# Optimization experiments

Hardware: AMD Instinct MI355X
Metric: run time of the kernel (lower is better)

## Reference

```python
import jax, jax.numpy as jnp
import numpy as np
from jax import lax

DIM = 64
HEADS = 8
B, H, W = 4, 256, 256


def layer_norm(x, w, b):
    # WithBias LayerNorm over channel dim (dim=1 of NCHW), per-pixel
    mu = jnp.mean(x, axis=1, keepdims=True)
    var = jnp.mean((x - mu) ** 2, axis=1, keepdims=True)
    xn = (x - mu) / jnp.sqrt(var + 1e-5)
    return xn * w[None, :, None, None] + b[None, :, None, None]


def conv1x1(x, w, b=None):
    out = jnp.einsum('oc,bchw->bohw', w, x)
    if b is not None:
        out = out + b[None, :, None, None]
    return out


def dwconv3x3(x, w):
    # w: [C,1,3,3], depthwise (groups=C), stride 1, pad 1
    return lax.conv_general_dilated(
        x, w, window_strides=(1, 1), padding=((1, 1), (1, 1)),
        feature_group_count=x.shape[1],
        dimension_numbers=('NCHW', 'OIHW', 'NCHW'))


def modulation(v, y, mw, mb):
    # mw: [4, C, C] = [scale0, scale1, shift0, shift1]; mb: [4, C]
    s = conv1x1(jax.nn.leaky_relu(conv1x1(y, mw[0], mb[0]), 0.1), mw[1], mb[1])
    t = conv1x1(jax.nn.leaky_relu(conv1x1(y, mw[2], mb[2]), 0.1), mw[3], mb[3])
    return v * (s + 1.0) + t


def _heads(t):
    b, c, h, w = t.shape
    return t.reshape(b, HEADS, c // HEADS, h * w)


def channel_attn(q, k, v, temp):
    b, c, h, w = v.shape
    q, k, v = _heads(q), _heads(k), _heads(v)  # b, head, ch, hw
    q = q / jnp.maximum(jnp.linalg.norm(q, axis=-1, keepdims=True), 1e-12)
    k = k / jnp.maximum(jnp.linalg.norm(k, axis=-1, keepdims=True), 1e-12)
    attn = jnp.einsum('bhcn,bhdn->bhcd', q, k) * temp[None]  # small CxC
    attn = jax.nn.softmax(attn, axis=-1)
    out = jnp.einsum('bhcd,bhdn->bhcn', attn, v)
    return out.reshape(b, c, h, w)


def setup_inputs() -> dict:
    key = jax.random.key(0)
    ks = jax.random.split(key, 24)
    sc = 0.05
    d = {
        'x': jax.random.normal(ks[0], (B, DIM, H, W), jnp.float32),
        'y': jax.random.normal(ks[1], (B, DIM, H, W), jnp.float32),
        'ln_w': jnp.ones((DIM,), jnp.float32),
        'ln_b': jnp.zeros((DIM,), jnp.float32),
        'temp': jnp.ones((HEADS, 1, 1), jnp.float32),
        'kv1_w': jax.random.normal(ks[2], (2 * DIM, DIM), jnp.float32) * sc,
        'kvdw1_w': jax.random.normal(ks[3], (2 * DIM, 1, 3, 3), jnp.float32) * sc,
        'q1_w': jax.random.normal(ks[4], (DIM, DIM), jnp.float32) * sc,
        'qdw1_w': jax.random.normal(ks[5], (DIM, 1, 3, 3), jnp.float32) * sc,
        'po1_w': jax.random.normal(ks[6], (DIM, DIM), jnp.float32) * sc,
        'kv2_w': jax.random.normal(ks[7], (2 * DIM, DIM), jnp.float32) * sc,
        'kvdw2_w': jax.random.normal(ks[8], (2 * DIM, 1, 3, 3), jnp.float32) * sc,
        'q2_w': jax.random.normal(ks[9], (DIM, DIM), jnp.float32) * sc,
        'qdw2_w': jax.random.normal(ks[10], (DIM, 1, 3, 3), jnp.float32) * sc,
        'po2_w': jax.random.normal(ks[11], (DIM, DIM), jnp.float32) * sc,
        'mm1_w': jax.random.normal(ks[12], (4, DIM, DIM), jnp.float32) * sc,
        'mm1_b': jnp.zeros((4, DIM), jnp.float32),
        'mm2_w': jax.random.normal(ks[13], (4, DIM, DIM), jnp.float32) * sc,
        'mm2_b': jnp.zeros((4, DIM), jnp.float32),
    }
    return d


def reference(x, y, ln_w, ln_b, temp,
              kv1_w, kvdw1_w, q1_w, qdw1_w, po1_w,
              kv2_w, kvdw2_w, q2_w, qdw2_w, po2_w,
              mm1_w, mm1_b, mm2_w, mm2_b):
    x1 = layer_norm(x, ln_w, ln_b)
    y1 = layer_norm(y, ln_w, ln_b)  # original reuses self.norm1 for both

    # branch 1: kv from x1, q from y1, v modulated by x, residual y
    kv1 = dwconv3x3(conv1x1(x1, kv1_w), kvdw1_w)
    k1, v1 = jnp.split(kv1, 2, axis=1)
    q1 = dwconv3x3(conv1x1(y1, q1_w), qdw1_w)
    v1 = modulation(v1, x, mm1_w, mm1_b)
    out1 = conv1x1(channel_attn(q1, k1, v1, temp), po1_w) + y

    # branch 2: kv from y1, q from x1, v modulated by y, residual x
    kv2 = dwconv3x3(conv1x1(y1, kv2_w), kvdw2_w)
    k2, v2 = jnp.split(kv2, 2, axis=1)
    q2 = dwconv3x3(conv1x1(x1, q2_w), qdw2_w)
    v2 = modulation(v2, y, mm2_w, mm2_b)
    out2 = conv1x1(channel_attn(q2, k2, v2, temp), po2_w) + x

    return (out1, out2)
```

## Files before the change

### kernel.cpp

```cpp
#include <hip/hip_runtime.h>
#include <hip/hip_bf16.h>

#define HW 65536
#define BATCH 4
#define NPIX (BATCH*HW)

typedef unsigned short u16;
typedef unsigned int   u32;
typedef __attribute__((ext_vector_type(8))) short bh8;
typedef __attribute__((ext_vector_type(4))) float f4;

__device__ __forceinline__ float b2f(u16 u){
    u32 i = ((u32)u) << 16; float f; __builtin_memcpy(&f, &i, 4); return f;
}
__device__ __forceinline__ u16 f2b(float f){
    __hip_bfloat16 h = __float2bfloat16(f); u16 u; __builtin_memcpy(&u, &h, 2); return u;
}

__device__ __forceinline__ f4 mfma16(bh8 a, bh8 b, f4 c){
    return __builtin_amdgcn_mfma_f32_16x16x32_bf16(a, b, c, 0, 0, 0);
}

struct CvtJob { const float* src; u16* dst; int n; const float* cs; };
struct CvtJobs { CvtJob j[12]; };
__global__ void cvt_kernel(CvtJobs jobs){
    const CvtJob J = jobs.j[blockIdx.x];
    if (J.cs){
        for (int i = threadIdx.x; i < J.n; i += 256) J.dst[i] = f2b(J.src[i] * J.cs[i & 63]);
    } else {
        for (int i = threadIdx.x; i < J.n; i += 256) J.dst[i] = f2b(J.src[i]);
    }
}

__global__ __launch_bounds__(256) void prep_kernel(const float* __restrict__ kv0w,
                                                   const float* __restrict__ kv1w,
                                                   const float* __restrict__ q0w,
                                                   const float* __restrict__ q1w,
                                                   const float* __restrict__ lnw,
                                                   const float* __restrict__ lnb,
                                                   float* __restrict__ sums,
                                                   float* __restrict__ lnc){
    int blk = blockIdx.x;
    if (blk == 0){
        for (int i = threadIdx.x; i < 5120; i += 256) sums[i] = 0.f;
    } else if (blk <= 2){
        const float* W = (blk == 1) ? kv0w : kv1w;
        float* rs = lnc + (blk-1)*256;
        int o = threadIdx.x;
        if (o < 128){
            float a = 0.f, bb = 0.f;
            for (int c = 0; c < 64; c++){
                float wv = W[o*64 + c];
                a = fmaf(wv, lnw[c], a); bb = fmaf(wv, lnb[c], bb);
            }
            rs[o] = a; rs[128 + o] = bb;
        }
    } else {
        const float* W = (blk == 3) ? q0w : q1w;
        float* rs = lnc + 512 + (blk-3)*128;
        int o = threadIdx.x;
        if (o < 64){
            float a = 0.f, bb = 0.f;
            for (int c = 0; c < 64; c++){
                float wv = W[o*64 + c];
                a = fmaf(wv, lnw[c], a); bb = fmaf(wv, lnb[c], bb);
            }
            rs[o] = a; rs[64 + o] = bb;
        }
    }
}

template<int MT, int KT, int EPI, typename TB, bool LNF>
__global__ __launch_bounds__(256) void gemm_kernel(
        const TB* __restrict__ inLo, const TB* __restrict__ inHi,
        const u16* __restrict__ WA,
        const float* __restrict__ rs, const float* __restrict__ rb,
        u16* __restrict__ outLo, u16* __restrict__ outHi,
        const float* __restrict__ resid, float* __restrict__ outF){
    constexpr int KD = KT*32;
    int tile = blockIdx.x;
    int w = threadIdx.x >> 6, lane = threadIdx.x & 63;
    int quad = lane >> 4, l16 = lane & 15;
    int b = tile >> 9;
    int pbase = ((tile & 511) << 7) + (w << 5) + (l16 << 1);

    bh8 a[MT][KT];
    const u16* wbase = (EPI == 3) ? (WA + b*4096) : WA;
    #pragma unroll
    for (int mi = 0; mi < MT; mi++){
        int row = mi*16 + l16;
        #pragma unroll
        for (int ks = 0; ks < KT; ks++)
            __builtin_memcpy(&a[mi][ks], wbase + row*KD + ks*32 + quad*8, 16);
    }
    f4 acc[MT][2];
    #pragma unroll
    for (int mi = 0; mi < MT; mi++){ acc[mi][0] = (f4){0.f,0.f,0.f,0.f}; acc[mi][1] = (f4){0.f,0.f,0.f,0.f}; }

    float s1a = 0.f, s2a = 0.f, s1b = 0.f, s2b = 0.f;
    #pragma unroll
    for (int ks = 0; ks < KT; ks++){
        int kblk = ks*32 + quad*8;
        const TB* base = (kblk < 64) ? inLo : inHi;
        const TB* pp = base + ((size_t)b*64 + (kblk & 63))*HW + pbase;
        bh8 b0, b1;
        #pragma unroll
        for (int j = 0; j < 8; j++){
            if constexpr (sizeof(TB) == 2){
                u32 m = *(const u32*)(pp + (size_t)j*HW);
                b0[j] = (short)(m & 0xffffu);
                b1[j] = (short)(m >> 16);
            } else {
                float2 f = *(const float2*)(pp + (size_t)j*HW);
                if constexpr (LNF){
                    s1a += f.x; s2a = fmaf(f.x, f.x, s2a);
                    s1b += f.y; s2b = fmaf(f.y, f.y, s2b);
                }
                b0[j] = (short)f2b(f.x);
                b1[j] = (short)f2b(f.y);
            }
        }
        #pragma unroll
        for (int mi = 0; mi < MT; mi++){
            acc[mi][0] = mfma16(a[mi][ks], b0, acc[mi][0]);
            acc[mi][1] = mfma16(a[mi][ks], b1, acc[mi][1]);
        }
    }

    float mu0 = 0.f, iv0 = 1.f, mu1 = 0.f, iv1 = 1.f;
    if constexpr (LNF){
        s1a += __shfl_xor(s1a, 16); s1a += __shfl_xor(s1a, 32);
        s2a += __shfl_xor(s2a, 16); s2a += __shfl_xor(s2a, 32);
        s1b += __shfl_xor(s1b, 16); s1b += __shfl_xor(s1b, 32);
        s2b += __shfl_xor(s2b, 16); s2b += __shfl_xor(s2b, 32);
        mu0 = s1a*(1.f/64.f); iv0 = rsqrtf(s2a*(1.f/64.f) - mu0*mu0 + 1e-5f);
        mu1 = s1b*(1.f/64.f); iv1 = rsqrtf(s2b*(1.f/64.f) - mu1*mu1 + 1e-5f);
    }

    #pragma unroll
    for (int mi = 0; mi < MT; mi++)
    #pragma unroll
    for (int r = 0; r < 4; r++){
        int o = mi*16 + quad*4 + r;
        size_t pidx = ((size_t)b*64 + (o & 63))*HW + pbase;
        float va0 = acc[mi][0][r];
        float va1 = acc[mi][1][r];
        if constexpr (EPI == 3){
            float2 rr = *(const float2*)(resid + pidx);
            float2 st; st.x = va0 + rr.x; st.y = va1 + rr.y;
            *(float2*)(outF + pidx) = st;
        } else {
            if constexpr (LNF){
                float rsv = rs[o], rbv = rb[o];
                va0 = iv0*(va0 - mu0*rsv) + rbv;
                va1 = iv1*(va1 - mu1*rsv) + rbv;
            }
            u16* dst = (o < 64) ? outLo : outHi;
            *(u32*)(dst + pidx) = (u32)f2b(va0) | ((u32)f2b(va1) << 16);
        }
    }
}

__global__ __launch_bounds__(256) void modfused_kernel(
        const float* __restrict__ in,
        const u16* __restrict__ WA, const u16* __restrict__ WB,
        const float* __restrict__ b0v, const float* __restrict__ b2v,
        const float* __restrict__ b1v, const float* __restrict__ b3v,
        u16* __restrict__ vP){
    __shared__ u32 lds[128*65];
    int tile = blockIdx.x;
    int w = threadIdx.x >> 6, lane = threadIdx.x & 63;
    int quad = lane >> 4, l16 = lane & 15;
    int b = tile >> 9;
    int pbase = ((tile & 511) << 7) + (w << 5) + (l16 << 1);
    int pxp = (w << 4) + l16;

    bh8 a1[8][2];
    #pragma unroll
    for (int mi = 0; mi < 8; mi++)
        #pragma unroll
        for (int ks = 0; ks < 2; ks++)
            __builtin_memcpy(&a1[mi][ks], WA + (mi*16+l16)*64 + ks*32 + quad*8, 16);
    f4 acc[8][2];
    #pragma unroll
    for (int mi = 0; mi < 8; mi++){ acc[mi][0] = (f4){0.f,0.f,0.f,0.f}; acc[mi][1] = (f4){0.f,0.f,0.f,0.f}; }
    #pragma unroll
    for (int ks = 0; ks < 2; ks++){
        const float* pp = in + ((size_t)b*64 + ks*32 + quad*8)*HW + pbase;
        bh8 f0, f1;
        #pragma unroll
        for (int j = 0; j < 8; j++){
            float2 f = *(const float2*)(pp + (size_t)j*HW);
            f0[j] = (short)f2b(f.x);
            f1[j] = (short)f2b(f.y);
        }
        #pragma unroll
        for (int mi = 0; mi < 8; mi++){
            acc[mi][0] = mfma16(a1[mi][ks], f0, acc[mi][0]);
            acc[mi][1] = mfma16(a1[mi][ks], f1, acc[mi][1]);
        }
    }
    #pragma unroll
    for (int mi = 0; mi < 8; mi++)
    #pragma unroll
    for (int r = 0; r < 4; r++){
        int o = mi*16 + quad*4 + r;
        float bi = (o < 64) ? b0v[o] : b2v[o-64];
        float v0 = acc[mi][0][r] + bi; v0 = v0 > 0.f ? v0 : 0.1f*v0;
        float v1 = acc[mi][1][r] + bi; v1 = v1 > 0.f ? v1 : 0.1f*v1;
        lds[o*65 + ((pxp + ((o>>2)&3)*4) & 63)] = (u32)f2b(v0) | ((u32)f2b(v1) << 16);
    }
    __syncthreads();

    bh8 a2[8][2];
    #pragma unroll
    for (int mi = 0; mi < 8; mi++)
        #pragma unroll
        for (int ks = 0; ks < 2; ks++)
            __builtin_memcpy(&a2[mi][ks], WB + (mi*16+l16)*64 + ks*32 + quad*8, 16);
    f4 acc2[8][2];
    #pragma unroll
    for (int mi = 0; mi < 8; mi++){ acc2[mi][0] = (f4){0.f,0.f,0.f,0.f}; acc2[mi][1] = (f4){0.f,0.f,0.f,0.f}; }
    #pragma unroll
    for (int ks = 0; ks < 4; ks++){
        int kb = ks*32 + quad*8;
        bh8 bb0, bb1;
        #pragma unroll
        for (int j = 0; j < 8; j++){
            int ch = kb + j;
            u32 m = lds[ch*65 + ((pxp + ((ch>>2)&3)*4) & 63)];
            bb0[j] = (short)(m & 0xffffu);
            bb1[j] = (short)(m >> 16);
        }
        #pragma unroll
        for (int mi = 0; mi < 8; mi++){
            if (mi < 4 ? (ks < 2) : (ks >= 2)){
                int ksl = (mi >= 4) ? ks - 2 : ks;
                acc2[mi][0] = mfma16(a2[mi][ksl], bb0, acc2[mi][0]);
                acc2[mi][1] = mfma16(a2[mi][ksl], bb1, acc2[mi][1]);
            }
        }
    }
    #pragma unroll
    for (int mi = 0; mi < 4; mi++)
    #pragma unroll
    for (int r = 0; r < 4; r++){
        int o = mi*16 + quad*4 + r;
        size_t pidx = ((size_t)b*64 + o)*HW + pbase;
        float s0 = acc2[mi][0][r] + b1v[o];
        float s1 = acc2[mi][1][r] + b1v[o];
        float t0 = acc2[mi+4][0][r] + b3v[o];
        float t1 = acc2[mi+4][1][r] + b3v[o];
        u32 vv = *(u32*)(vP + pidx);
        float v0 = b2f((u16)(vv & 0xffffu)), v1 = b2f((u16)(vv >> 16));
        *(u32*)(vP + pidx) = (u32)f2b(v0*(s0+1.f)+t0)
                           | ((u32)f2b(v1*(s1+1.f)+t1) << 16);
    }
}

struct DwArgs { const u16* in0; const u16* in1; const u16* in2;
                u16* out0; u16* out1; u16* out2;
                const float* w0; const float* w1; const float* w2;
                int c0, c1, c2; };
__global__ __launch_bounds__(256) void dw3_kernel(DwArgs A){
    int seg = blockIdx.x >> 13;
    int lid = ((blockIdx.x & 8191) << 8) + threadIdx.x;
    const u16* inp = seg == 0 ? A.in0 : seg == 1 ? A.in1 : A.in2;
    u16* outp      = seg == 0 ? A.out0 : seg == 1 ? A.out1 : A.out2;
    const float* wd = seg == 0 ? A.w0 : seg == 1 ? A.w1 : A.w2;
    int choff      = seg == 0 ? A.c0 : seg == 1 ? A.c1 : A.c2;
    int bc = lid >> 13;
    int n8 = lid & 8191;
    int h = n8 >> 5, c8 = (n8 & 31) << 3;
    const float* wc = wd + ((size_t)((bc & 63) + choff))*9;
    const u16* p = inp + (size_t)bc*HW;
    float row[3][10];
    #pragma unroll
    for (int r = 0; r < 3; r++){
        int hh = h - 1 + r;
        bool ok = (unsigned)hh < 256u;
        const u16* pr = p + hh*256 + c8;
        if (ok){
            uint4 m = *(const uint4*)pr;
            row[r][1] = b2f((u16)m.x); row[r][2] = b2f((u16)(m.x>>16));
            row[r][3] = b2f((u16)m.y); row[r][4] = b2f((u16)(m.y>>16));
            row[r][5] = b2f((u16)m.z); row[r][6] = b2f((u16)(m.z>>16));
            row[r][7] = b2f((u16)m.w); row[r][8] = b2f((u16)(m.w>>16));
            row[r][0] = (c8 > 0)   ? b2f(pr[-1]) : 0.f;
            row[r][9] = (c8 < 248) ? b2f(pr[8])  : 0.f;
        } else {
            #pragma unroll
            for (int j = 0; j < 10; j++) row[r][j] = 0.f;
        }
    }
    float o[8];
    #pragma unroll
    for (int i = 0; i < 8; i++){
        float a = 0.f;
        #pragma unroll
        for (int r = 0; r < 3; r++){
            a = fmaf(wc[r*3+0], row[r][i],   a);
            a = fmaf(wc[r*3+1], row[r][i+1], a);
            a = fmaf(wc[r*3+2], row[r][i+2], a);
        }
        o[i] = a;
    }
    uint4 st;
    st.x = (u32)f2b(o[0]) | ((u32)f2b(o[1])<<16);
    st.y = (u32)f2b(o[2]) | ((u32)f2b(o[3])<<16);
    st.z = (u32)f2b(o[4]) | ((u32)f2b(o[5])<<16);
    st.w = (u32)f2b(o[6]) | ((u32)f2b(o[7])<<16);
    *(uint4*)(outp + (size_t)bc*HW + h*256 + c8) = st;
}

#define NSL 64
__global__ __launch_bounds__(256) void attn_part_kernel(const u16* __restrict__ q,
                                                        const u16* __restrict__ k,
                                                        float* __restrict__ sums){
    int blk = blockIdx.x;
    int sl = blk & (NSL-1);
    int bh = blk >> 6;
    int b = bh >> 3, h = bh & 7;
    const u16* qp = q + ((size_t)b*64 + h*8)*HW + sl*(HW/NSL);
    const u16* kp = k + ((size_t)b*64 + h*8)*HW + sl*(HW/NSL);
    float acc[80];
    #pragma unroll
    for (int i = 0; i < 80; i++) acc[i] = 0.f;
    int n0 = threadIdx.x << 2;
    float qv[8][4], kw[8][4];
    #pragma unroll
    for (int i = 0; i < 8; i++){
        uint2 mq = *(const uint2*)(qp + (size_t)i*HW + n0);
        uint2 mk = *(const uint2*)(kp + (size_t)i*HW + n0);
        qv[i][0] = b2f((u16)(mq.x & 0xffffu)); qv[i][1] = b2f((u16)(mq.x >> 16));
        qv[i][2] = b2f((u16)(mq.y & 0xffffu)); qv[i][3] = b2f((u16)(mq.y >> 16));
        kw[i][0] = b2f((u16)(mk.x & 0xffffu)); kw[i][1] = b2f((u16)(mk.x >> 16));
        kw[i][2] = b2f((u16)(mk.y & 0xffffu)); kw[i][3] = b2f((u16)(mk.y >> 16));
    }
    #pragma unroll
    for (int i = 0; i < 8; i++){
        #pragma unroll
        for (int u = 0; u < 4; u++){
            acc[64+i] = fmaf(qv[i][u], qv[i][u], acc[64+i]);
            acc[72+i] = fmaf(kw[i][u], kw[i][u], acc[72+i]);
        }
        #pragma unroll
        for (int j = 0; j < 8; j++)
            #pragma unroll
            for (int u = 0; u < 4; u++)
                acc[i*8+j] = fmaf(qv[i][u], kw[j][u], acc[i*8+j]);
    }
    __shared__ float sred[4][80];
    int lane = threadIdx.x & 63, wv = threadIdx.x >> 6;
    #pragma unroll
    for (int t = 0; t < 80; t++){
        float r = acc[t];
        r += __shfl_down(r, 32); r += __shfl_down(r, 16); r += __shfl_down(r, 8);
        r += __shfl_down(r, 4);  r += __shfl_down(r, 2);  r += __shfl_down(r, 1);
        if (lane == 0) sred[wv][t] = r;
    }
    __syncthreads();
    if (threadIdx.x < 80){
        int t = threadIdx.x;
        atomicAdd(&sums[bh*80 + t], sred[0][t]+sred[1][t]+sred[2][t]+sred[3][t]);
    }
}

__global__ __launch_bounds__(64) void weff_kernel(const float* __restrict__ sums,
                                                  const float* __restrict__ temp,
                                                  const float* __restrict__ po,
                                                  u16* __restrict__ weff){
    int b = blockIdx.x;
    __shared__ float at[8][8][8];
    int t = threadIdx.x;
    {
        int h = t >> 3, i = t & 7;
        const float* f = sums + (b*8 + h)*80;
        float iq = 1.f / fmaxf(sqrtf(f[64+i]), 1e-12f);
        float tv = temp[h];
        float row[8]; float m = -1e30f;
        #pragma unroll
        for (int j = 0; j < 8; j++){
            float ik = 1.f / fmaxf(sqrtf(f[72+j]), 1e-12f);
            row[j] = f[i*8+j]*iq*ik*tv;
            m = fmaxf(m, row[j]);
        }
        float s = 0.f;
        #pragma unroll
        for (int j = 0; j < 8; j++){ row[j] = expf(row[j]-m); s += row[j]; }
        float rs = 1.f/s;
        #pragma unroll
        for (int j = 0; j < 8; j++) at[h][i][j] = row[j]*rs;
    }
    __syncthreads();
    int o = t;
    for (int g = 0; g < 64; g++){
        int h = g >> 3, j = g & 7;
        float wv = 0.f;
        #pragma unroll
        for (int i = 0; i < 8; i++) wv = fmaf(po[o*64 + h*8 + i], at[h][i][j], wv);
        weff[b*4096 + o*64 + g] = f2b(wv);
    }
}

extern "C" void kernel_launch(void* const* d_in, const int* in_sizes, int n_in,
                              void* d_out, int out_size, void* d_ws, size_t ws_size,
                              hipStream_t stream){
    const float* x    = (const float*)d_in[0];
    const float* y    = (const float*)d_in[1];
    const float* ln_w = (const float*)d_in[2];
    const float* ln_b = (const float*)d_in[3];
    const float* temp = (const float*)d_in[4];
    const float* kv_w[2]   = {(const float*)d_in[5],  (const float*)d_in[10]};
    const float* kvdw_w[2] = {(const float*)d_in[6],  (const float*)d_in[11]};
    const float* q_w[2]    = {(const float*)d_in[7],  (const float*)d_in[12]};
    const float* qdw_w[2]  = {(const float*)d_in[8],  (const float*)d_in[13]};
    const float* po_w[2]   = {(const float*)d_in[9],  (const float*)d_in[14]};
    const float* mm_w[2]   = {(const float*)d_in[15], (const float*)d_in[17]};
    const float* mm_b[2]   = {(const float*)d_in[16], (const float*)d_in[18]};

    const size_t HPE = (size_t)BATCH*64*HW;
    u16* PL = (u16*)d_ws;
    u16* P0 = PL;            u16* P1 = PL +   HPE;
    u16* P2 = PL + 2*HPE;    u16* P3 = PL + 3*HPE;
    u16* P4 = PL + 4*HPE;    u16* P5 = PL + 5*HPE;
    float* sums = (float*)(PL + 6*HPE);
    float* lnc  = sums + 5120;
    u16* warena = (u16*)(lnc + 768);
    const int WKV[2] = {0, 8192}, WQ[2] = {16384, 20480};
    const int WMA[2] = {24576, 40960}, WMB[2] = {32768, 49152};
    const int WEFF = 57344;

    size_t need = 6*HPE*2 + (5120+768)*4 + 73728*2;
    if (ws_size < need) return;

    CvtJobs jobs{}; int nj = 0;
    auto add = [&](const float* s, u16* d, int n, const float* cs){ jobs.j[nj] = {s, d, n, cs}; nj++; };
    for (int br = 0; br < 2; br++){
        add(kv_w[br],        warena + WKV[br],        8192, ln_w);
        add(q_w[br],         warena + WQ[br],         4096, ln_w);
        add(mm_w[br],        warena + WMA[br],        4096, nullptr);
        add(mm_w[br]+8192,   warena + WMA[br] + 4096, 4096, nullptr);
        add(mm_w[br]+4096,   warena + WMB[br],        4096, nullptr);
        add(mm_w[br]+12288,  warena + WMB[br] + 4096, 4096, nullptr);
    }
    cvt_kernel<<<nj, 256, 0, stream>>>(jobs);
    prep_kernel<<<5, 256, 0, stream>>>(kv_w[0], kv_w[1], q_w[0], q_w[1],
                                       ln_w, ln_b, sums, lnc);

    float* outp = (float*)d_out;
    const int GT = NPIX/128;
    for (int br = 0; br < 2; br++){
        const float* in_kv  = br==0 ? x  : y;
        const float* in_q   = br==0 ? y  : x;
        const float* mod_in = br==0 ? x  : y;
        const float* resid  = br==0 ? y  : x;
        float* sb = sums + br*2560;
        const float* rs_kv = lnc + br*256;
        const float* rs_q  = lnc + 512 + br*128;

        gemm_kernel<8,2,0,float,true><<<GT, 256, 0, stream>>>(
            in_kv, in_kv, warena + WKV[br], rs_kv, rs_kv+128, P0, P1, nullptr, nullptr);
        gemm_kernel<4,2,0,float,true><<<GT, 256, 0, stream>>>(
            in_q, in_q, warena + WQ[br], rs_q, rs_q+64, P2, P2, nullptr, nullptr);
        DwArgs da{P0, P1, P2, P3, P4, P5,
                  kvdw_w[br], kvdw_w[br], qdw_w[br], 0, 64, 0};
        dw3_kernel<<<3*8192, 256, 0, stream>>>(da);
        modfused_kernel<<<GT, 256, 0, stream>>>(
            mod_in, warena + WMA[br], warena + WMB[br],
            mm_b[br], mm_b[br]+128, mm_b[br]+64, mm_b[br]+192, P4);
        attn_part_kernel<<<BATCH*8*NSL, 256, 0, stream>>>(P5, P3, sb);
        weff_kernel<<<BATCH, 64, 0, stream>>>(sb, temp, po_w[br], warena + WEFF);
        gemm_kernel<4,2,3,u16,false><<<GT, 256, 0, stream>>>(
            P4, P4, warena + WEFF, nullptr, nullptr, nullptr, nullptr,
            resid, outp + (size_t)br*HPE);
    }
}
```

Baseline: 760.3 us.

## Batch both branches per launch and fuse modulation with output projection

Merges the two branches into single launches (setup, dual GEMM+LN, attention partials, weff) and fuses the modulation MLP with the final projection and residual. The modulated v no longer makes a round trip through global memory, and the weights are staged in swizzled LDS instead of per-thread registers. This removes launches and about a third of the intermediate HBM traffic. The costs are more workspace buffers and more LDS per block in the fused kernel, which could reduce occupancy.

```diff
diff --git a/kernel.cpp b/kernel.cpp
--- a/kernel.cpp
+++ b/kernel.cpp
@@ -22,239 +22,126 @@
 }
 
 struct CvtJob { const float* src; u16* dst; int n; const float* cs; };
-struct CvtJobs { CvtJob j[12]; };
-__global__ void cvt_kernel(CvtJobs jobs){
-    const CvtJob J = jobs.j[blockIdx.x];
-    if (J.cs){
-        for (int i = threadIdx.x; i < J.n; i += 256) J.dst[i] = f2b(J.src[i] * J.cs[i & 63]);
-    } else {
-        for (int i = threadIdx.x; i < J.n; i += 256) J.dst[i] = f2b(J.src[i]);
-    }
-}
-
-__global__ __launch_bounds__(256) void prep_kernel(const float* __restrict__ kv0w,
-                                                   const float* __restrict__ kv1w,
-                                                   const float* __restrict__ q0w,
-                                                   const float* __restrict__ q1w,
-                                                   const float* __restrict__ lnw,
-                                                   const float* __restrict__ lnb,
-                                                   float* __restrict__ sums,
-                                                   float* __restrict__ lnc){
+struct SetupArgs {
+    CvtJob j[12];
+    const float* kvw[2]; const float* qw[2];
+    const float* lnw; const float* lnb;
+    float* sums; float* lnc;
+};
+__global__ __launch_bounds__(256) void setup_kernel(SetupArgs S){
     int blk = blockIdx.x;
-    if (blk == 0){
-        for (int i = threadIdx.x; i < 5120; i += 256) sums[i] = 0.f;
-    } else if (blk <= 2){
-        const float* W = (blk == 1) ? kv0w : kv1w;
-        float* rs = lnc + (blk-1)*256;
+    if (blk < 12){
+        const CvtJob J = S.j[blk];
+        if (J.cs){
+            for (int i = threadIdx.x; i < J.n; i += 256) J.dst[i] = f2b(J.src[i] * J.cs[i & 63]);
+        } else {
+            for (int i = threadIdx.x; i < J.n; i += 256) J.dst[i] = f2b(J.src[i]);
+        }
+        return;
+    }
+    int pb = blk - 12;
+    if (pb == 0){
+        for (int i = threadIdx.x; i < 5120; i += 256) S.sums[i] = 0.f;
+    } else if (pb <= 2){
+        const float* W = S.kvw[pb-1];
+        float* rs = S.lnc + (pb-1)*256;
         int o = threadIdx.x;
         if (o < 128){
             float a = 0.f, bb = 0.f;
             for (int c = 0; c < 64; c++){
                 float wv = W[o*64 + c];
-                a = fmaf(wv, lnw[c], a); bb = fmaf(wv, lnb[c], bb);
+                a = fmaf(wv, S.lnw[c], a); bb = fmaf(wv, S.lnb[c], bb);
             }
             rs[o] = a; rs[128 + o] = bb;
         }
     } else {
-        const float* W = (blk == 3) ? q0w : q1w;
-        float* rs = lnc + 512 + (blk-3)*128;
+        const float* W = S.qw[pb-3];
+        float* rs = S.lnc + 512 + (pb-3)*128;
         int o = threadIdx.x;
         if (o < 64){
             float a = 0.f, bb = 0.f;
             for (int c = 0; c < 64; c++){
                 float wv = W[o*64 + c];
-                a = fmaf(wv, lnw[c], a); bb = fmaf(wv, lnb[c], bb);
+                a = fmaf(wv, S.lnw[c], a); bb = fmaf(wv, S.lnb[c], bb);
             }
             rs[o] = a; rs[64 + o] = bb;
         }
     }
 }
 
-template<int MT, int KT, int EPI, typename TB, bool LNF>
-__global__ __launch_bounds__(256) void gemm_kernel(
-        const TB* __restrict__ inLo, const TB* __restrict__ inHi,
-        const u16* __restrict__ WA,
-        const float* __restrict__ rs, const float* __restrict__ rb,
-        u16* __restrict__ outLo, u16* __restrict__ outHi,
-        const float* __restrict__ resid, float* __restrict__ outF){
-    constexpr int KD = KT*32;
-    int tile = blockIdx.x;
+struct GemmDual {
+    const float* in[2];
+    const u16* wa[2];
+    const float* rs[2]; const float* rb[2];
+    u16* outLo[2]; u16* outHi[2];
+};
+template<int MT>
+__global__ __launch_bounds__(256,4) void gemmln_kernel(GemmDual G){
+    constexpr int KD = 64;
+    constexpr int NW = MT*16*KD;
+    __shared__ u16 wl[NW];
+    int seg = blockIdx.x >> 11, tile = blockIdx.x & 2047;
+    {
+        const u16* W = G.wa[seg];
+        for (int i = threadIdx.x; i < NW/8; i += 256){
+            int row = i >> 3, ch = i & 7;
+            uint4 v = *(const uint4*)(W + row*KD + ch*8);
+            *(uint4*)(wl + row*KD + ((ch ^ (row & 7)) << 3)) = v;
+        }
+    }
+    __syncthreads();
+
     int w = threadIdx.x >> 6, lane = threadIdx.x & 63;
     int quad = lane >> 4, l16 = lane & 15;
     int b = tile >> 9;
     int pbase = ((tile & 511) << 7) + (w << 5) + (l16 << 1);
 
-    bh8 a[MT][KT];
-    const u16* wbase = (EPI == 3) ? (WA + b*4096) : WA;
-    #pragma unroll
-    for (int mi = 0; mi < MT; mi++){
-        int row = mi*16 + l16;
-        #pragma unroll
-        for (int ks = 0; ks < KT; ks++)
-            __builtin_memcpy(&a[mi][ks], wbase + row*KD + ks*32 + quad*8, 16);
-    }
     f4 acc[MT][2];
     #pragma unroll
     for (int mi = 0; mi < MT; mi++){ acc[mi][0] = (f4){0.f,0.f,0.f,0.f}; acc[mi][1] = (f4){0.f,0.f,0.f,0.f}; }
 
     float s1a = 0.f, s2a = 0.f, s1b = 0.f, s2b = 0.f;
     #pragma unroll
-    for (int ks = 0; ks < KT; ks++){
-        int kblk = ks*32 + quad*8;
-        const TB* base = (kblk < 64) ? inLo : inHi;
-        const TB* pp = base + ((size_t)b*64 + (kblk & 63))*HW + pbase;
+    for (int ks = 0; ks < 2; ks++){
+        const float* pp = G.in[seg] + ((size_t)b*64 + ks*32 + quad*8)*HW + pbase;
         bh8 b0, b1;
         #pragma unroll
         for (int j = 0; j < 8; j++){
-            if constexpr (sizeof(TB) == 2){
-                u32 m = *(const u32*)(pp + (size_t)j*HW);
-                b0[j] = (short)(m & 0xffffu);
-                b1[j] = (short)(m >> 16);
-            } else {
-                float2 f = *(const float2*)(pp + (size_t)j*HW);
-                if constexpr (LNF){
-                    s1a += f.x; s2a = fmaf(f.x, f.x, s2a);
-                    s1b += f.y; s2b = fmaf(f.y, f.y, s2b);
-                }
-                b0[j] = (short)f2b(f.x);
-                b1[j] = (short)f2b(f.y);
-            }
+            float2 f = *(const float2*)(pp + (size_t)j*HW);
+            s1a += f.x; s2a = fmaf(f.x, f.x, s2a);
+            s1b += f.y; s2b = fmaf(f.y, f.y, s2b);
+            b0[j] = (short)f2b(f.x);
+            b1[j] = (short)f2b(f.y);
         }
         #pragma unroll
         for (int mi = 0; mi < MT; mi++){
-            acc[mi][0] = mfma16(a[mi][ks], b0, acc[mi][0]);
-            acc[mi][1] = mfma16(a[mi][ks], b1, acc[mi][1]);
-        }
-    }
-
-    float mu0 = 0.f, iv0 = 1.f, mu1 = 0.f, iv1 = 1.f;
-    if constexpr (LNF){
-        s1a += __shfl_xor(s1a, 16); s1a += __shfl_xor(s1a, 32);
-        s2a += __shfl_xor(s2a, 16); s2a += __shfl_xor(s2a, 32);
-        s1b += __shfl_xor(s1b, 16); s1b += __shfl_xor(s1b, 32);
-        s2b += __shfl_xor(s2b, 16); s2b += __shfl_xor(s2b, 32);
-        mu0 = s1a*(1.f/64.f); iv0 = rsqrtf(s2a*(1.f/64.f) - mu0*mu0 + 1e-5f);
-        mu1 = s1b*(1.f/64.f); iv1 = rsqrtf(s2b*(1.f/64.f) - mu1*mu1 + 1e-5f);
-    }
-
+            bh8 a;
+            __builtin_memcpy(&a, wl + (mi*16 + l16)*KD + ((((ks<<2)+quad) ^ (l16 & 7)) << 3), 16);
+            acc[mi][0] = mfma16(a, b0, acc[mi][0]);
+            acc[mi][1] = mfma16(a, b1, acc[mi][1]);
+        }
+    }
+
+    s1a += __shfl_xor(s1a, 16); s1a += __shfl_xor(s1a, 32);
+    s2a += __shfl_xor(s2a, 16); s2a += __shfl_xor(s2a, 32);
+    s1b += __shfl_xor(s1b, 16); s1b += __shfl_xor(s1b, 32);
+    s2b += __shfl_xor(s2b, 16); s2b += __shfl_xor(s2b, 32);
+    float mu0 = s1a*(1.f/64.f), iv0 = rsqrtf(s2a*(1.f/64.f) - mu0*mu0 + 1e-5f);
+    float mu1 = s1b*(1.f/64.f), iv1 = rsqrtf(s2b*(1.f/64.f) - mu1*mu1 + 1e-5f);
+
+    const float* rs = G.rs[seg]; const float* rb = G.rb[seg];
+    u16* oLo = G.outLo[seg]; u16* oHi = G.outHi[seg];
     #pragma unroll
     for (int mi = 0; mi < MT; mi++)
     #pragma unroll
     for (int r = 0; r < 4; r++){
         int o = mi*16 + quad*4 + r;
         size_t pidx = ((size_t)b*64 + (o & 63))*HW + pbase;
-        float va0 = acc[mi][0][r];
-        float va1 = acc[mi][1][r];
-        if constexpr (EPI == 3){
-            float2 rr = *(const float2*)(resid + pidx);
-            float2 st; st.x = va0 + rr.x; st.y = va1 + rr.y;
-            *(float2*)(outF + pidx) = st;
-        } else {
-            if constexpr (LNF){
-                float rsv = rs[o], rbv = rb[o];
-                va0 = iv0*(va0 - mu0*rsv) + rbv;
-                va1 = iv1*(va1 - mu1*rsv) + rbv;
-            }
-            u16* dst = (o < 64) ? outLo : outHi;
-            *(u32*)(dst + pidx) = (u32)f2b(va0) | ((u32)f2b(va1) << 16);
-        }
-    }
-}
-
-__global__ __launch_bounds__(256) void modfused_kernel(
-        const float* __restrict__ in,
-        const u16* __restrict__ WA, const u16* __restrict__ WB,
-        const float* __restrict__ b0v, const float* __restrict__ b2v,
-        const float* __restrict__ b1v, const float* __restrict__ b3v,
-        u16* __restrict__ vP){
-    __shared__ u32 lds[128*65];
-    int tile = blockIdx.x;
-    int w = threadIdx.x >> 6, lane = threadIdx.x & 63;
-    int quad = lane >> 4, l16 = lane & 15;
-    int b = tile >> 9;
-    int pbase = ((tile & 511) << 7) + (w << 5) + (l16 << 1);
-    int pxp = (w << 4) + l16;
-
-    bh8 a1[8][2];
-    #pragma unroll
-    for (int mi = 0; mi < 8; mi++)
-        #pragma unroll
-        for (int ks = 0; ks < 2; ks++)
-            __builtin_memcpy(&a1[mi][ks], WA + (mi*16+l16)*64 + ks*32 + quad*8, 16);
-    f4 acc[8][2];
-    #pragma unroll
-    for (int mi = 0; mi < 8; mi++){ acc[mi][0] = (f4){0.f,0.f,0.f,0.f}; acc[mi][1] = (f4){0.f,0.f,0.f,0.f}; }
-    #pragma unroll
-    for (int ks = 0; ks < 2; ks++){
-        const float* pp = in + ((size_t)b*64 + ks*32 + quad*8)*HW + pbase;
-        bh8 f0, f1;
-        #pragma unroll
-        for (int j = 0; j < 8; j++){
-            float2 f = *(const float2*)(pp + (size_t)j*HW);
-            f0[j] = (short)f2b(f.x);
-            f1[j] = (short)f2b(f.y);
-        }
-        #pragma unroll
-        for (int mi = 0; mi < 8; mi++){
-            acc[mi][0] = mfma16(a1[mi][ks], f0, acc[mi][0]);
-            acc[mi][1] = mfma16(a1[mi][ks], f1, acc[mi][1]);
-        }
-    }
-    #pragma unroll
-    for (int mi = 0; mi < 8; mi++)
-    #pragma unroll
-    for (int r = 0; r < 4; r++){
-        int o = mi*16 + quad*4 + r;
-        float bi = (o < 64) ? b0v[o] : b2v[o-64];
-        float v0 = acc[mi][0][r] + bi; v0 = v0 > 0.f ? v0 : 0.1f*v0;
-        float v1 = acc[mi][1][r] + bi; v1 = v1 > 0.f ? v1 : 0.1f*v1;
-        lds[o*65 + ((pxp + ((o>>2)&3)*4) & 63)] = (u32)f2b(v0) | ((u32)f2b(v1) << 16);
-    }
-    __syncthreads();
-
-    bh8 a2[8][2];
-    #pragma unroll
-    for (int mi = 0; mi < 8; mi++)
-        #pragma unroll
-        for (int ks = 0; ks < 2; ks++)
-            __builtin_memcpy(&a2[mi][ks], WB + (mi*16+l16)*64 + ks*32 + quad*8, 16);
-    f4 acc2[8][2];
-    #pragma unroll
-    for (int mi = 0; mi < 8; mi++){ acc2[mi][0] = (f4){0.f,0.f,0.f,0.f}; acc2[mi][1] = (f4){0.f,0.f,0.f,0.f}; }
-    #pragma unroll
-    for (int ks = 0; ks < 4; ks++){
-        int kb = ks*32 + quad*8;
-        bh8 bb0, bb1;
-        #pragma unroll
-        for (int j = 0; j < 8; j++){
-            int ch = kb + j;
-            u32 m = lds[ch*65 + ((pxp + ((ch>>2)&3)*4) & 63)];
-            bb0[j] = (short)(m & 0xffffu);
-            bb1[j] = (short)(m >> 16);
-        }
-        #pragma unroll
-        for (int mi = 0; mi < 8; mi++){
-            if (mi < 4 ? (ks < 2) : (ks >= 2)){
-                int ksl = (mi >= 4) ? ks - 2 : ks;
-                acc2[mi][0] = mfma16(a2[mi][ksl], bb0, acc2[mi][0]);
-                acc2[mi][1] = mfma16(a2[mi][ksl], bb1, acc2[mi][1]);
-            }
-        }
-    }
-    #pragma unroll
-    for (int mi = 0; mi < 4; mi++)
-    #pragma unroll
-    for (int r = 0; r < 4; r++){
-        int o = mi*16 + quad*4 + r;
-        size_t pidx = ((size_t)b*64 + o)*HW + pbase;
-        float s0 = acc2[mi][0][r] + b1v[o];
-        float s1 = acc2[mi][1][r] + b1v[o];
-        float t0 = acc2[mi+4][0][r] + b3v[o];
-        float t1 = acc2[mi+4][1][r] + b3v[o];
-        u32 vv = *(u32*)(vP + pidx);
-        float v0 = b2f((u16)(vv & 0xffffu)), v1 = b2f((u16)(vv >> 16));
-        *(u32*)(vP + pidx) = (u32)f2b(v0*(s0+1.f)+t0)
-                           | ((u32)f2b(v1*(s1+1.f)+t1) << 16);
+        float rsv = rs[o], rbv = rb[o];
+        float va0 = iv0*(acc[mi][0][r] - mu0*rsv) + rbv;
+        float va1 = iv1*(acc[mi][1][r] - mu1*rsv) + rbv;
+        u16* dst = (o < 64) ? oLo : oHi;
+        *(u32*)(dst + pidx) = (u32)f2b(va0) | ((u32)f2b(va1) << 16);
     }
 }
 
@@ -314,15 +201,15 @@
 }
 
 #define NSL 64
-__global__ __launch_bounds__(256) void attn_part_kernel(const u16* __restrict__ q,
-                                                        const u16* __restrict__ k,
-                                                        float* __restrict__ sums){
-    int blk = blockIdx.x;
+struct AttnDual { const u16* q[2]; const u16* k[2]; float* sums; };
+__global__ __launch_bounds__(256) void attn_part_kernel(AttnDual AD){
+    int seg = blockIdx.x >> 11;
+    int blk = blockIdx.x & 2047;
     int sl = blk & (NSL-1);
     int bh = blk >> 6;
     int b = bh >> 3, h = bh & 7;
-    const u16* qp = q + ((size_t)b*64 + h*8)*HW + sl*(HW/NSL);
-    const u16* kp = k + ((size_t)b*64 + h*8)*HW + sl*(HW/NSL);
+    const u16* qp = AD.q[seg] + ((size_t)b*64 + h*8)*HW + sl*(HW/NSL);
+    const u16* kp = AD.k[seg] + ((size_t)b*64 + h*8)*HW + sl*(HW/NSL);
     float acc[80];
     #pragma unroll
     for (int i = 0; i < 80; i++) acc[i] = 0.f;
@@ -362,22 +249,23 @@
     __syncthreads();
     if (threadIdx.x < 80){
         int t = threadIdx.x;
-        atomicAdd(&sums[bh*80 + t], sred[0][t]+sred[1][t]+sred[2][t]+sred[3][t]);
-    }
-}
-
-__global__ __launch_bounds__(64) void weff_kernel(const float* __restrict__ sums,
-                                                  const float* __restrict__ temp,
-                                                  const float* __restrict__ po,
-                                                  u16* __restrict__ weff){
-    int b = blockIdx.x;
+        atomicAdd(&AD.sums[seg*2560 + bh*80 + t], sred[0][t]+sred[1][t]+sred[2][t]+sred[3][t]);
+    }
+}
+
+struct WeffDual { const float* sums; const float* temp; const float* po[2]; u16* weff[2]; };
+__global__ __launch_bounds__(64) void weff_kernel(WeffDual WD){
+    int seg = blockIdx.x >> 2;
+    int b = blockIdx.x & 3;
+    const float* po = WD.po[seg];
+    u16* weff = WD.weff[seg];
     __shared__ float at[8][8][8];
     int t = threadIdx.x;
     {
         int h = t >> 3, i = t & 7;
-        const float* f = sums + (b*8 + h)*80;
+        const float* f = WD.sums + seg*2560 + (b*8 + h)*80;
         float iq = 1.f / fmaxf(sqrtf(f[64+i]), 1e-12f);
-        float tv = temp[h];
+        float tv = WD.temp[h];
         float row[8]; float m = -1e30f;
         #pragma unroll
         for (int j = 0; j < 8; j++){
@@ -388,9 +276,9 @@
         float s = 0.f;
         #pragma unroll
         for (int j = 0; j < 8; j++){ row[j] = expf(row[j]-m); s += row[j]; }
-        float rs = 1.f/s;
-        #pragma unroll
-        for (int j = 0; j < 8; j++) at[h][i][j] = row[j]*rs;
+        float rsv = 1.f/s;
+        #pragma unroll
+        for (int j = 0; j < 8; j++) at[h][i][j] = row[j]*rsv;
     }
     __syncthreads();
     int o = t;
@@ -400,6 +288,159 @@
         #pragma unroll
         for (int i = 0; i < 8; i++) wv = fmaf(po[o*64 + h*8 + i], at[h][i][j], wv);
         weff[b*4096 + o*64 + g] = f2b(wv);
+    }
+}
+
+struct ModFinal {
+    const float* in[2]; const u16* wa[2]; const u16* wb[2];
+    const float* b0[2]; const float* b2[2]; const float* b1[2]; const float* b3[2];
+    const u16* wf[2];
+    const u16* v[2];
+    const float* resid[2];
+    float* out[2];
+};
+__global__ __launch_bounds__(256) void modfinal_kernel(ModFinal M){
+    __shared__ u32 lds[128*65];
+    __shared__ u16 wl[8192];
+    int seg = blockIdx.x >> 11, tile = blockIdx.x & 2047;
+    int w = threadIdx.x >> 6, lane = threadIdx.x & 63;
+    int quad = lane >> 4, l16 = lane & 15;
+    int b = tile >> 9;
+    int pbase = ((tile & 511) << 7) + (w << 5) + (l16 << 1);
+    int pxp = (w << 4) + l16;
+
+    auto loadW = [&](const u16* W, int nrows){
+        for (int i = threadIdx.x; i < nrows*8; i += 256){
+            int row = i >> 3, ch = i & 7;
+            uint4 vv = *(const uint4*)(W + row*64 + ch*8);
+            *(uint4*)(wl + row*64 + ((ch ^ (row & 7)) << 3)) = vv;
+        }
+    };
+
+    loadW(M.wa[seg], 128);
+    __syncthreads();
+    f4 acc[8][2];
+    #pragma unroll
+    for (int mi = 0; mi < 8; mi++){ acc[mi][0] = (f4){0.f,0.f,0.f,0.f}; acc[mi][1] = (f4){0.f,0.f,0.f,0.f}; }
+    #pragma unroll
+    for (int ks = 0; ks < 2; ks++){
+        const float* pp = M.in[seg] + ((size_t)b*64 + ks*32 + quad*8)*HW + pbase;
+        bh8 f0, f1;
+        #pragma unroll
+        for (int j = 0; j < 8; j++){
+            float2 f = *(const float2*)(pp + (size_t)j*HW);
+            f0[j] = (short)f2b(f.x);
+            f1[j] = (short)f2b(f.y);
+        }
+        #pragma unroll
+        for (int mi = 0; mi < 8; mi++){
+            bh8 a;
+            __builtin_memcpy(&a, wl + (mi*16 + l16)*64 + ((((ks<<2)+quad) ^ (l16 & 7)) << 3), 16);
+            acc[mi][0] = mfma16(a, f0, acc[mi][0]);
+            acc[mi][1] = mfma16(a, f1, acc[mi][1]);
+        }
+    }
+    {
+        const float* b0v = M.b0[seg]; const float* b2v = M.b2[seg];
+        #pragma unroll
+        for (int mi = 0; mi < 8; mi++)
+        #pragma unroll
+        for (int r = 0; r < 4; r++){
+            int o = mi*16 + quad*4 + r;
+            float bi = (o < 64) ? b0v[o] : b2v[o-64];
+            float v0 = acc[mi][0][r] + bi; v0 = v0 > 0.f ? v0 : 0.1f*v0;
+            float v1 = acc[mi][1][r] + bi; v1 = v1 > 0.f ? v1 : 0.1f*v1;
+            lds[o*65 + ((pxp + ((o>>2)&3)*4) & 63)] = (u32)f2b(v0) | ((u32)f2b(v1) << 16);
+        }
+    }
+    __syncthreads();
+
+    loadW(M.wb[seg], 128);
+    __syncthreads();
+    f4 acc2[8][2];
+    #pragma unroll
+    for (int mi = 0; mi < 8; mi++){ acc2[mi][0] = (f4){0.f,0.f,0.f,0.f}; acc2[mi][1] = (f4){0.f,0.f,0.f,0.f}; }
+    #pragma unroll
+    for (int ks = 0; ks < 4; ks++){
+        int kb = ks*32 + quad*8;
+        bh8 bb0, bb1;
+        #pragma unroll
+        for (int j = 0; j < 8; j++){
+            int ch = kb + j;
+            u32 m = lds[ch*65 + ((pxp + ((ch>>2)&3)*4) & 63)];
+            bb0[j] = (short)(m & 0xffffu);
+            bb1[j] = (short)(m >> 16);
+        }
+        #pragma unroll
+        for (int mi = 0; mi < 8; mi++){
+            if (mi < 4 ? (ks < 2) : (ks >= 2)){
+                int ksl = (mi >= 4) ? ks - 2 : ks;
+                bh8 a;
+                __builtin_memcpy(&a, wl + (mi*16 + l16)*64 + ((((ksl<<2)+quad) ^ (l16 & 7)) << 3), 16);
+                acc2[mi][0] = mfma16(a, bb0, acc2[mi][0]);
+                acc2[mi][1] = mfma16(a, bb1, acc2[mi][1]);
+            }
+        }
+    }
+    __syncthreads();
+
+    loadW(M.wf[seg] + b*4096, 64);
+    {
+        const float* b1v = M.b1[seg]; const float* b3v = M.b3[seg];
+        const u16* vP = M.v[seg];
+        #pragma unroll
+        for (int mi = 0; mi < 4; mi++)
+        #pragma unroll
+        for (int r = 0; r < 4; r++){
+            int o = mi*16 + quad*4 + r;
+            size_t pidx = ((size_t)b*64 + o)*HW + pbase;
+            float s0 = acc2[mi][0][r] + b1v[o];
+            float s1 = acc2[mi][1][r] + b1v[o];
+            float t0 = acc2[mi+4][0][r] + b3v[o];
+            float t1 = acc2[mi+4][1][r] + b3v[o];
+            u32 vv = *(const u32*)(vP + pidx);
+            float v0 = b2f((u16)(vv & 0xffffu)), v1 = b2f((u16)(vv >> 16));
+            lds[o*65 + ((pxp + ((o>>2)&3)*4) & 63)] = (u32)f2b(v0*(s0+1.f)+t0)
+                                                    | ((u32)f2b(v1*(s1+1.f)+t1) << 16);
+        }
+    }
+    __syncthreads();
+
+    f4 accF[4][2];
+    #pragma unroll
+    for (int mi = 0; mi < 4; mi++){ accF[mi][0] = (f4){0.f,0.f,0.f,0.f}; accF[mi][1] = (f4){0.f,0.f,0.f,0.f}; }
+    #pragma unroll
+    for (int ks = 0; ks < 2; ks++){
+        int kb = ks*32 + quad*8;
+        bh8 bb0, bb1;
+        #pragma unroll
+        for (int j = 0; j < 8; j++){
+            int ch = kb + j;
+            u32 m = lds[ch*65 + ((pxp + ((ch>>2)&3)*4) & 63)];
+            bb0[j] = (short)(m & 0xffffu);
+            bb1[j] = (short)(m >> 16);
+        }
+        #pragma unroll
+        for (int mi = 0; mi < 4; mi++){
+            bh8 a;
+            __builtin_memcpy(&a, wl + (mi*16 + l16)*64 + ((((ks<<2)+quad) ^ (l16 & 7)) << 3), 16);
+            accF[mi][0] = mfma16(a, bb0, accF[mi][0]);
+            accF[mi][1] = mfma16(a, bb1, accF[mi][1]);
+        }
+    }
+    {
+        const float* resid = M.resid[seg];
+        float* outF = M.out[seg];
+        #pragma unroll
+        for (int mi = 0; mi < 4; mi++)
+        #pragma unroll
+        for (int r = 0; r < 4; r++){
+            int o = mi*16 + quad*4 + r;
+            size_t pidx = ((size_t)b*64 + o)*HW + pbase;
+            float2 rr = *(const float2*)(resid + pidx);
+            float2 st; st.x = accF[mi][0][r] + rr.x; st.y = accF[mi][1][r] + rr.y;
+            *(float2*)(outF + pidx) = st;
+        }
     }
 }
 
@@ -421,21 +462,21 @@
 
     const size_t HPE = (size_t)BATCH*64*HW;
     u16* PL = (u16*)d_ws;
-    u16* P0 = PL;            u16* P1 = PL +   HPE;
-    u16* P2 = PL + 2*HPE;    u16* P3 = PL + 3*HPE;
-    u16* P4 = PL + 4*HPE;    u16* P5 = PL + 5*HPE;
-    float* sums = (float*)(PL + 6*HPE);
+    u16* P[9];
+    for (int i = 0; i < 9; i++) P[i] = PL + (size_t)i*HPE;
+    float* sums = (float*)(PL + 9*HPE);
     float* lnc  = sums + 5120;
     u16* warena = (u16*)(lnc + 768);
     const int WKV[2] = {0, 8192}, WQ[2] = {16384, 20480};
     const int WMA[2] = {24576, 40960}, WMB[2] = {32768, 49152};
-    const int WEFF = 57344;
-
-    size_t need = 6*HPE*2 + (5120+768)*4 + 73728*2;
+    const int WEFF[2] = {57344, 73728};
+
+    size_t need = 9*HPE*2 + (5120+768)*4 + 90112*2;
     if (ws_size < need) return;
 
-    CvtJobs jobs{}; int nj = 0;
-    auto add = [&](const float* s, u16* d, int n, const float* cs){ jobs.j[nj] = {s, d, n, cs}; nj++; };
+    SetupArgs S{};
+    int nj = 0;
+    auto add = [&](const float* s, u16* d, int n, const float* cs){ S.j[nj] = {s, d, n, cs}; nj++; };
     for (int br = 0; br < 2; br++){
         add(kv_w[br],        warena + WKV[br],        8192, ln_w);
         add(q_w[br],         warena + WQ[br],         4096, ln_w);
@@ -444,35 +485,62 @@
         add(mm_w[br]+4096,   warena + WMB[br],        4096, nullptr);
         add(mm_w[br]+12288,  warena + WMB[br] + 4096, 4096, nullptr);
     }
-    cvt_kernel<<<nj, 256, 0, stream>>>(jobs);
-    prep_kernel<<<5, 256, 0, stream>>>(kv_w[0], kv_w[1], q_w[0], q_w[1],
-                                       ln_w, ln_b, sums, lnc);
+    S.kvw[0] = kv_w[0]; S.kvw[1] = kv_w[1];
+    S.qw[0]  = q_w[0];  S.qw[1]  = q_w[1];
+    S.lnw = ln_w; S.lnb = ln_b; S.sums = sums; S.lnc = lnc;
+    setup_kernel<<<17, 256, 0, stream>>>(S);
+
+    const int GT = NPIX/128;
+
+    GemmDual GK{};
+    GK.in[0] = x; GK.in[1] = y;
+    GK.wa[0] = warena + WKV[0]; GK.wa[1] = warena + WKV[1];
+    GK.rs[0] = lnc;        GK.rb[0] = lnc + 128;
+    GK.rs[1] = lnc + 256;  GK.rb[1] = lnc + 384;
+    GK.outLo[0] = P[0]; GK.outHi[0] = P[1];
+    GK.outLo[1] = P[3]; GK.outHi[1] = P[4];
+    gemmln_kernel<8><<<2*GT, 256, 0, stream>>>(GK);
+
+    GemmDual GQ{};
+    GQ.in[0] = y; GQ.in[1] = x;
+    GQ.wa[0] = warena + WQ[0]; GQ.wa[1] = warena + WQ[1];
+    GQ.rs[0] = lnc + 512;  GQ.rb[0] = lnc + 576;
+    GQ.rs[1] = lnc + 640;  GQ.rb[1] = lnc + 704;
+    GQ.outLo[0] = P[2]; GQ.outHi[0] = P[2];
+    GQ.outLo[1] = P[5]; GQ.outHi[1] = P[5];
+    gemmln_kernel<4><<<2*GT, 256, 0, stream>>>(GQ);
+
+    DwArgs D0{P[0], P[1], P[2], P[6], P[7], P[8],
+              kvdw_w[0], kvdw_w[0], qdw_w[0], 0, 64, 0};
+    dw3_kernel<<<3*8192, 256, 0, stream>>>(D0);
+    DwArgs D1{P[3], P[4], P[5], P[0], P[1], P[2],
+              kvdw_w[1], kvdw_w[1], qdw_w[1], 0, 64, 0};
+    dw3_kernel<<<3*8192, 256, 0, stream>>>(D1);
+
+    AttnDual AD{};
+    AD.q[0] = P[8]; AD.k[0] = P[6];
+    AD.q[1] = P[2]; AD.k[1] = P[0];
+    AD.sums = sums;
+    attn_part_kernel<<<2*BATCH*8*NSL, 256, 0, stream>>>(AD);
+
+    WeffDual WD{};
+    WD.sums = sums; WD.temp = temp;
+    WD.po[0] = po_w[0]; WD.po[1] = po_w[1];
+    WD.weff[0] = warena + WEFF[0]; WD.weff[1] = warena + WEFF[1];
+    weff_kernel<<<2*BATCH, 64, 0, stream>>>(WD);
 
     float* outp = (float*)d_out;
-    const int GT = NPIX/128;
-    for (int br = 0; br < 2; br++){
-        const float* in_kv  = br==0 ? x  : y;
-        const float* in_q   = br==0 ? y  : x;
-        const float* mod_in = br==0 ? x  : y;
-        const float* resid  = br==0 ? y  : x;
-        float* sb = sums + br*2560;
-        const float* rs_kv = lnc + br*256;
-        const float* rs_q  = lnc + 512 + br*128;
-
-        gemm_kernel<8,2,0,float,true><<<GT, 256, 0, stream>>>(
-            in_kv, in_kv, warena + WKV[br], rs_kv, rs_kv+128, P0, P1, nullptr, nullptr);
-        gemm_kernel<4,2,0,float,true><<<GT, 256, 0, stream>>>(
-            in_q, in_q, warena + WQ[br], rs_q, rs_q+64, P2, P2, nullptr, nullptr);
-        DwArgs da{P0, P1, P2, P3, P4, P5,
-                  kvdw_w[br], kvdw_w[br], qdw_w[br], 0, 64, 0};
-        dw3_kernel<<<3*8192, 256, 0, stream>>>(da);
-        modfused_kernel<<<GT, 256, 0, stream>>>(
-            mod_in, warena + WMA[br], warena + WMB[br],
-            mm_b[br], mm_b[br]+128, mm_b[br]+64, mm_b[br]+192, P4);
-        attn_part_kernel<<<BATCH*8*NSL, 256, 0, stream>>>(P5, P3, sb);
-        weff_kernel<<<BATCH, 64, 0, stream>>>(sb, temp, po_w[br], warena + WEFF);
-        gemm_kernel<4,2,3,u16,false><<<GT, 256, 0, stream>>>(
-            P4, P4, warena + WEFF, nullptr, nullptr, nullptr, nullptr,
-            resid, outp + (size_t)br*HPE);
-    }
-}
+    ModFinal M{};
+    M.in[0] = x; M.in[1] = y;
+    M.wa[0] = warena + WMA[0]; M.wa[1] = warena + WMA[1];
+    M.wb[0] = warena + WMB[0]; M.wb[1] = warena + WMB[1];
+    M.b0[0] = mm_b[0];       M.b0[1] = mm_b[1];
+    M.b2[0] = mm_b[0] + 128; M.b2[1] = mm_b[1] + 128;
+    M.b1[0] = mm_b[0] + 64;  M.b1[1] = mm_b[1] + 64;
+    M.b3[0] = mm_b[0] + 192; M.b3[1] = mm_b[1] + 192;
+    M.wf[0] = warena + WEFF[0]; M.wf[1] = warena + WEFF[1];
+    M.v[0] = P[7]; M.v[1] = P[1];
+    M.resid[0] = y; M.resid[1] = x;
+    M.out[0] = outp; M.out[1] = outp + HPE;
+    modfinal_kernel<<<2*GT, 256, 0, stream>>>(M);
+}
```

Measured after the change: 741.5 us. 2.5% less time.
